# Kernel optimization log

Measured on AMD Instinct MI355X. Metric: run time of the kernel, lower is better.

Reference implementation:

```python
import jax, jax.numpy as jnp
import numpy as np

MIN_NORM = 1e-15
EPS = 1e-7          # fp32 eps used by hgcn Hyperboloid
MAX_NORM = 1e6
C = 1.0             # curvature for all layers (args.c = 1)
N, D = 16384, 64

# ---- Hyperboloid manifold ops (faithful to hgcn manifolds/hyperboloid.py) ----

def _norm(v):
    return jnp.sqrt(jnp.sum(v * v, axis=-1, keepdims=True))

def proj(x, c):
    K = 1.0 / c
    y = x[..., 1:]
    x0 = jnp.sqrt(jnp.clip(K + jnp.sum(y * y, -1, keepdims=True), EPS))
    return jnp.concatenate([x0, y], -1)

def proj_tan0(u, c):
    return jnp.concatenate([jnp.zeros_like(u[..., :1]), u[..., 1:]], -1)

def expmap0(u, c):
    sqrtK = (1.0 / c) ** 0.5
    x = u[..., 1:]
    xn = jnp.clip(_norm(x), MIN_NORM)
    theta = xn / sqrtK
    res = jnp.concatenate([sqrtK * jnp.cosh(theta),
                           sqrtK * jnp.sinh(theta) * x / xn], -1)
    return proj(res, c)

def logmap0(x, c):
    sqrtK = (1.0 / c) ** 0.5
    y = x[..., 1:]
    yn = jnp.clip(_norm(y), MIN_NORM)
    theta = jnp.clip(x[..., :1] / sqrtK, 1.0 + EPS)
    return jnp.concatenate([jnp.zeros_like(theta),
                            sqrtK * jnp.arccosh(theta) * y / yn], -1)

def mink_dot(x, y):
    return -x[..., :1] * y[..., :1] + jnp.sum(x[..., 1:] * y[..., 1:], -1, keepdims=True)

def expmap(u, x, c):
    sqrtK = (1.0 / c) ** 0.5
    normu = jnp.minimum(jnp.sqrt(jnp.clip(mink_dot(u, u), EPS)), MAX_NORM)
    theta = jnp.clip(normu / sqrtK, MIN_NORM)
    return proj(jnp.cosh(theta) * x + jnp.sinh(theta) * u / theta, c)

def proj_tan(u, x, c):
    ux = jnp.sum(x[..., 1:] * u[..., 1:], -1, keepdims=True)
    return jnp.concatenate([ux / jnp.clip(x[..., :1], EPS), u[..., 1:]], -1)

def ptransp0(x, u, c):
    sqrtK = (1.0 / c) ** 0.5
    x0, y = x[..., :1], x[..., 1:]
    yn = jnp.clip(_norm(y), MIN_NORM)
    yhat = y / yn
    v = jnp.concatenate([-yn, (sqrtK - x0) * yhat], -1)
    alpha = jnp.sum(yhat * u[..., 1:], -1, keepdims=True) / sqrtK
    return proj_tan(u - alpha * v, x, c)

def mobius_add(x, y, c):
    u = logmap0(y, c)
    v = ptransp0(x, u, c)
    return expmap(v, x, c)

# ---- HGCN layers (HypLinear -> HypAgg -> HypAct), dropout=0, use_att=False ----

def hyp_linear(x, W, b, c):
    mv = expmap0(logmap0(x, c) @ W.T, c)   # mobius_matvec
    res = proj(mv, c)
    hyp_bias = proj(expmap0(proj_tan0(b[None, :], c), c), c)
    return proj(mobius_add(res, hyp_bias, c), c)

def hyp_agg(x, adj_n, c):
    return proj(expmap0(adj_n @ logmap0(x, c), c), c)

def hyp_act(x, c_in, c_out):
    xt = proj_tan0(jax.nn.relu(logmap0(x, c_in)), c_out)
    return proj(expmap0(xt, c_out), c_out)

def hgc_layer(x, adj_n, W, b, c_in, c_out):
    h = hyp_linear(x, W, b, c_in)
    h = hyp_agg(h, adj_n, c_in)
    return hyp_act(h, c_in, c_out)

def setup_inputs() -> dict:
    key = jax.random.key(0)
    k1, k2, k3, k4, k5, k6 = jax.random.split(key, 6)
    return {
        "x": jax.random.normal(k1, (N, D), jnp.float32),
        "adj": jax.random.uniform(k2, (N, N), jnp.float32),
        "W1": jax.random.normal(k3, (D, D), jnp.float32) * 0.125,
        "b1": jax.random.normal(k4, (D,), jnp.float32) * 0.01,
        "W2": jax.random.normal(k5, (D, D), jnp.float32) * 0.125,
        "b2": jax.random.normal(k6, (D,), jnp.float32) * 0.01,
    }

def reference(x, adj, W1, b1, W2, b2):
    # project input to hyperboloid
    x_hyp = proj(expmap0(proj_tan0(x, C), C), C)
    # row-normalize adjacency: D^{-1} A (inf -> 0)
    rsum = jnp.sum(adj, axis=1)
    rinv = jnp.where(rsum != 0, 1.0 / rsum, 0.0)
    adj_n = rinv[:, None] * adj
    h1 = hgc_layer(x_hyp, adj_n, W1, b1, C, C)
    h2 = hgc_layer(h1, adj_n, W2, b2, C, C)
    return (h1, h2)
```

## Files before the change

### kernel.cpp

```cpp
#include <hip/hip_runtime.h>
#include <cstdint>
#include <cstddef>

#define NROWS 16384
#define KDIM  16384
#define EPSF  1e-7f
#define MINN  1e-15f
#define MAXN  1e6f
#define KSPLIT 8
#define KRANGE (KDIM/KSPLIT)
#define BM    64
#define BK    64
#define NSTEP (KRANGE/BK)
#define APGS  528
#define BPGS  520
#define ABUF  (8*APGS)
#define BBUF  (8*BPGS)

typedef __attribute__((ext_vector_type(16))) float f32x16;
typedef long long i64;
typedef unsigned long long u64;
typedef unsigned int uint;

__device__ __forceinline__ float wredsum(float v){
  v += __shfl_xor(v, 1);
  v += __shfl_xor(v, 2);
  v += __shfl_xor(v, 4);
  v += __shfl_xor(v, 8);
  v += __shfl_xor(v, 16);
  v += __shfl_xor(v, 32);
  return v;
}

__global__ __launch_bounds__(128) void k_bias(const float* __restrict__ b1,
                                              const float* __restrict__ b2,
                                              float* __restrict__ ub){
  int w = threadIdx.x >> 6, l = threadIdx.x & 63;
  const float* b = w ? b2 : b1;
  float bv = b[l];
  float tb = l ? bv : 0.f;
  float s  = wredsum(tb*tb);
  float xn = fmaxf(sqrtf(s), MINN);
  float sc = sinhf(xn)/xn;
  float e  = sc*tb;
  float s2 = wredsum(e*e);
  float x0 = sqrtf(fmaxf(1.f+s2, EPSF));
  float yn = fmaxf(sqrtf(s2), MINN);
  float th = fmaxf(x0, 1.f+EPSF);
  float u  = l ? acoshf(th)*e/yn : 0.f;
  ub[w*64 + l] = u;
}

__global__ __launch_bounds__(256) void k_cvt(const float* __restrict__ adj,
                                             uint* __restrict__ adjF8,
                                             float* __restrict__ rinv){
  int tid  = threadIdx.x;
  int lane = tid & 63;
  int row  = blockIdx.x*4 + (tid >> 6);
  const float4* src = (const float4*)(adj + (size_t)row*KDIM);
  uint* dst = adjF8 + (size_t)row*(KDIM/4);
  float rs = 0.f;
  #pragma unroll 8
  for(int it = 0; it < KDIM/256; it++){
    float4 v = src[it*64 + lane];
    rs += (v.x + v.y) + (v.z + v.w);
    uint p = __builtin_amdgcn_cvt_pk_fp8_f32(v.x, v.y, 0u, false);
    p = __builtin_amdgcn_cvt_pk_fp8_f32(v.z, v.w, p, true);
    dst[it*64 + lane] = p;
  }
  rs = wredsum(rs);
  if (lane == 0) rinv[row] = (rs != 0.f) ? 1.f/rs : 0.f;
}

template<int MODE>
__global__ __launch_bounds__(256) void k_linear(const float* __restrict__ in,
                                                const float* __restrict__ W,
                                                const float* __restrict__ ub,
                                                float* __restrict__ g){
  __shared__ float Wt[64*65];
  int tid = threadIdx.x;
  for(int idx = tid; idx < 4096; idx += 256){
    int j = idx >> 6, k = idx & 63;
    Wt[k*65 + j] = W[idx];
  }
  __syncthreads();
  int lane = tid & 63;
  int row  = blockIdx.x*4 + (tid >> 6);
  float v = in[(size_t)row*64 + lane];
  float lx;
  if (MODE == 0){
    float t  = lane ? v : 0.f;
    float s  = wredsum(t*t);
    float tn = fmaxf(sqrtf(s), MINN);
    float sc = sinhf(tn)/tn;
    float e  = sc*t;
    float s2 = wredsum(e*e);
    float x0 = sqrtf(fmaxf(1.f+s2, EPSF));
    float yn = fmaxf(sqrtf(s2), MINN);
    float th = fmaxf(x0, 1.f+EPSF);
    lx = lane ? acoshf(th)*e/yn : 0.f;
  } else {
    float t  = lane ? v : 0.f;
    float s2 = wredsum(t*t);
    float x0 = __shfl(v, 0);
    float yn = fmaxf(sqrtf(s2), MINN);
    float th = fmaxf(x0, 1.f+EPSF);
    lx = lane ? acoshf(th)*t/yn : 0.f;
  }
  float mv = 0.f;
  #pragma unroll
  for(int k = 0; k < 64; k++){
    mv = fmaf(__shfl(lx, k), Wt[k*65 + lane], mv);
  }
  float u  = lane ? mv : 0.f;
  float s  = wredsum(u*u);
  float un = fmaxf(sqrtf(s), MINN);
  float sc = sinhf(un)/un;
  float e  = sc*u;
  float s2 = wredsum(e*e);
  float r0 = sqrtf(fmaxf(1.f+s2, EPSF));
  float ubt   = lane ? ub[lane] : 0.f;
  float yn    = fmaxf(sqrtf(s2), MINN);
  float yhat  = e/yn;
  float alpha = wredsum(yhat*ubt);
  float w     = ubt - alpha*(1.f - r0)*yhat;
  float ux    = wredsum(e*w);
  float v0    = ux / fmaxf(r0, EPSF);
  float md    = wredsum(w*w) - v0*v0;
  float normu = fminf(sqrtf(fmaxf(md, EPSF)), MAXN);
  float th2   = fmaxf(normu, MINN);
  float ch    = coshf(th2);
  float shq   = sinhf(th2)/th2;
  float ov    = ch*(lane ? e : r0) + shq*(lane ? w : v0);
  float ot    = lane ? ov : 0.f;
  float s3    = wredsum(ot*ot);
  float o0    = sqrtf(fmaxf(1.f+s3, EPSF));
  float yn2 = fmaxf(sqrtf(s3), MINN);
  float th3 = fmaxf(o0, 1.f+EPSF);
  float gv  = lane ? acoshf(th3)*ot/yn2 : 0.f;
  g[(size_t)row*64 + lane] = gv;
}

__global__ __launch_bounds__(256) void k_trf8(const float* __restrict__ g,
                                              uint* __restrict__ gF8T){
  __shared__ float t[64][65];
  int tid = threadIdx.x;
  int b   = blockIdx.x;
  int r   = tid >> 2;
  int c0  = (tid & 3)*16;
  const float* src = g + ((size_t)b*64 + r)*64 + c0;
  #pragma unroll
  for(int i = 0; i < 4; i++){
    float4 v = *(const float4*)(src + i*4);
    t[r][c0 + i*4 + 0] = v.x; t[r][c0 + i*4 + 1] = v.y;
    t[r][c0 + i*4 + 2] = v.z; t[r][c0 + i*4 + 3] = v.w;
  }
  __syncthreads();
  int n   = tid >> 2;
  int seg = tid & 3;
  int s16 = seg*16;
  uint4 p;
  p.x = __builtin_amdgcn_cvt_pk_fp8_f32(t[s16+ 0][n], t[s16+ 1][n], 0u, false);
  p.x = __builtin_amdgcn_cvt_pk_fp8_f32(t[s16+ 2][n], t[s16+ 3][n], p.x, true);
  p.y = __builtin_amdgcn_cvt_pk_fp8_f32(t[s16+ 4][n], t[s16+ 5][n], 0u, false);
  p.y = __builtin_amdgcn_cvt_pk_fp8_f32(t[s16+ 6][n], t[s16+ 7][n], p.y, true);
  p.z = __builtin_amdgcn_cvt_pk_fp8_f32(t[s16+ 8][n], t[s16+ 9][n], 0u, false);
  p.z = __builtin_amdgcn_cvt_pk_fp8_f32(t[s16+10][n], t[s16+11][n], p.z, true);
  p.w = __builtin_amdgcn_cvt_pk_fp8_f32(t[s16+12][n], t[s16+13][n], 0u, false);
  p.w = __builtin_amdgcn_cvt_pk_fp8_f32(t[s16+14][n], t[s16+15][n], p.w, true);
  uint4* dst = (uint4*)gF8T + (size_t)n*(KDIM/16) + b*4 + seg;
  *dst = p;
}

__global__ __launch_bounds__(256) void k_matmul(const unsigned char* __restrict__ adjF8,
                                                const unsigned char* __restrict__ gF8T,
                                                float* __restrict__ pagg){
  __shared__ __align__(16) char Alds[2*ABUF];
  __shared__ __align__(16) char Blds[2*BBUF];
  int tid  = threadIdx.x;
  int lane = tid & 63, w = tid >> 6;
  int rb   = blockIdx.x;
  int ks   = blockIdx.y;
  int row0 = rb*BM;
  size_t k0 = (size_t)ks * KRANGE;

  int sr   = tid >> 2;
  int sseg = tid & 3;
  const uint4* ap = (const uint4*)(adjF8 + (size_t)(row0 + sr)*KDIM + k0 + sseg*16);
  int AwOff0 = (2*sseg    )*APGS + sr*8;
  int AwOff1 = (2*sseg + 1)*APGS + sr*8;

  int sc  = tid >> 2;
  int skq = tid & 3;
  const uint4* bsp = (const uint4*)(gF8T + (size_t)sc*KDIM + k0 + skq*16);
  int BwOff0 = (2*skq    )*BPGS + sc*8;
  int BwOff1 = (2*skq + 1)*BPGS + sc*8;

  int wm = w >> 1, wn = w & 1;
  int lr = lane & 31, lh = lane >> 5;
  int ArdOff = lh*APGS + (wm*32 + lr)*8;
  int BrdOff = lh*BPGS + (wn*32 + lr)*8;

  f32x16 acc;
  #pragma unroll
  for(int q = 0; q < 16; q++) acc[q] = 0.f;

  uint4 aR, aN, bR, bN;

  aR = ap[0];
  bR = bsp[0];
  {
    union { uint4 v; u64 q[2]; } ua; ua.v = aR;
    *(u64*)(Alds + AwOff0) = ua.q[0];
    *(u64*)(Alds + AwOff1) = ua.q[1];
    union { uint4 v; u64 q[2]; } ub_; ub_.v = bR;
    *(u64*)(Blds + BwOff0) = ub_.q[0];
    *(u64*)(Blds + BwOff1) = ub_.q[1];
  }
  aR = ap[4];
  bR = bsp[4];
  __syncthreads();

  for (int i = 0; i < NSTEP; i++){
    const char* Ab = Alds + (i & 1)*ABUF;
    const char* Bb = Blds + (i & 1)*BBUF;
    i64 af0 = *(const i64*)(Ab + ArdOff);
    i64 af1 = *(const i64*)(Ab + ArdOff + 2*APGS);
    i64 af2 = *(const i64*)(Ab + ArdOff + 4*APGS);
    i64 af3 = *(const i64*)(Ab + ArdOff + 6*APGS);
    i64 bf0 = *(const i64*)(Bb + BrdOff);
    i64 bf1 = *(const i64*)(Bb + BrdOff + 2*BPGS);
    i64 bf2 = *(const i64*)(Bb + BrdOff + 4*BPGS);
    i64 bf3 = *(const i64*)(Bb + BrdOff + 6*BPGS);
    if (i + 2 < NSTEP){
      aN = ap[(i+2)*4];
      bN = bsp[(i+2)*4];
    }
    acc = __builtin_amdgcn_mfma_f32_32x32x16_fp8_fp8(af0, bf0, acc, 0, 0, 0);
    acc = __builtin_amdgcn_mfma_f32_32x32x16_fp8_fp8(af1, bf1, acc, 0, 0, 0);
    acc = __builtin_amdgcn_mfma_f32_32x32x16_fp8_fp8(af2, bf2, acc, 0, 0, 0);
    acc = __builtin_amdgcn_mfma_f32_32x32x16_fp8_fp8(af3, bf3, acc, 0, 0, 0);
    if (i + 1 < NSTEP){
      char* Aw = Alds + ((i+1) & 1)*ABUF;
      char* Bw = Blds + ((i+1) & 1)*BBUF;
      union { uint4 v; u64 q[2]; } ua; ua.v = aR;
      *(u64*)(Aw + AwOff0) = ua.q[0];
      *(u64*)(Aw + AwOff1) = ua.q[1];
      union { uint4 v; u64 q[2]; } ub_; ub_.v = bR;
      *(u64*)(Bw + BwOff0) = ub_.q[0];
      *(u64*)(Bw + BwOff1) = ub_.q[1];
    }
    aR = aN; bR = bN;
    __syncthreads();
  }

  float* ob = pagg + ((size_t)ks*NROWS + row0 + wm*32)*64 + wn*32;
  #pragma unroll
  for(int q = 0; q < 16; q++){
    int rl = (q & 3) + 8*(q >> 2) + 4*lh;
    ob[(size_t)rl*64 + lr] = acc[q];
  }
}

__global__ __launch_bounds__(256) void k_post(const float* __restrict__ pagg,
                                              const float* __restrict__ rinv,
                                              float* __restrict__ h){
  int tid = threadIdx.x; int lane = tid & 63;
  int row = blockIdx.x*4 + (tid >> 6);
  float s = 0.f;
  #pragma unroll
  for(int ks = 0; ks < KSPLIT; ks++) s += pagg[(size_t)ks*NROWS*64 + (size_t)row*64 + lane];
  float a  = s * rinv[row];
  float at = lane ? a : 0.f;
  float ss = wredsum(at*at);
  float un = fmaxf(sqrtf(ss), MINN);
  float sc = sinhf(un)/un;
  float e  = sc*at;
  float s2 = wredsum(e*e);
  float x0 = sqrtf(fmaxf(1.f+s2, EPSF));
  float yn = fmaxf(sqrtf(s2), MINN);
  float th = fmaxf(x0, 1.f+EPSF);
  float lt = lane ? acoshf(th)*e/yn : 0.f;
  float rl = fmaxf(lt, 0.f);
  float s3 = wredsum(rl*rl);
  float rn = fmaxf(sqrtf(s3), MINN);
  float sc2= sinhf(rn)/rn;
  float e2 = sc2*rl;
  float s4 = wredsum(e2*e2);
  float h0 = sqrtf(fmaxf(1.f+s4, EPSF));
  h[(size_t)row*64 + lane] = lane ? e2 : h0;
}

extern "C" void kernel_launch(void* const* d_in, const int* in_sizes, int n_in,
                              void* d_out, int out_size, void* d_ws, size_t ws_size,
                              hipStream_t stream){
  const float* x   = (const float*)d_in[0];
  const float* adj = (const float*)d_in[1];
  const float* W1  = (const float*)d_in[2];
  const float* b1  = (const float*)d_in[3];
  const float* W2  = (const float*)d_in[4];
  const float* b2  = (const float*)d_in[5];
  float* out = (float*)d_out;
  float* h1  = out;
  float* h2  = out + (size_t)NROWS*64;

  float* wsf   = (float*)d_ws;
  float* gbuf  = wsf;
  float* pagg  = gbuf  + (size_t)NROWS*64;
  float* rinv  = pagg  + (size_t)KSPLIT*NROWS*64;
  float* ubs   = rinv  + NROWS;
  uint*  gF8T  = (uint*)(ubs + 128);
  uint*  adjF8 = gF8T + (size_t)64*KDIM/4;

  dim3 gm(NROWS/BM, KSPLIT);

  k_bias<<<1, 128, 0, stream>>>(b1, b2, ubs);
  k_cvt<<<NROWS/4, 256, 0, stream>>>(adj, adjF8, rinv);
  k_linear<0><<<NROWS/4, 256, 0, stream>>>(x, W1, ubs, gbuf);
  k_trf8<<<NROWS/64, 256, 0, stream>>>(gbuf, gF8T);
  k_matmul<<<gm, 256, 0, stream>>>((const unsigned char*)adjF8, (const unsigned char*)gF8T, pagg);
  k_post<<<NROWS/4, 256, 0, stream>>>(pagg, rinv, h1);
  k_linear<1><<<NROWS/4, 256, 0, stream>>>(h1, W2, ubs + 64, gbuf);
  k_trf8<<<NROWS/64, 256, 0, stream>>>(gbuf, gF8T);
  k_matmul<<<gm, 256, 0, stream>>>((const unsigned char*)adjF8, (const unsigned char*)gF8T, pagg);
  k_post<<<NROWS/4, 256, 0, stream>>>(pagg, rinv, h2);
}
```

Before: 521.9 us.

## Fuse fp32-to-fp8 adjacency conversion and row sums into first aggregation matmul

Removes the standalone conversion kernel. The first matmul now reads fp32 adjacency directly, converts each tile to fp8 in registers, writes the fp8 copy out for reuse by the second layer, and accumulates partial row sums. The first post kernel reduces these partial sums to get the row normalizers. The second matmul walks its blocks in reverse order, so it starts on the adjacency tiles the first one touched last and may still find them in cache. This saves one full pass reading the 1 GB fp32 adjacency, but puts conversion work and larger fp32 loads inside the matmul's pipeline.

```diff
diff --git a/kernel.cpp b/kernel.cpp
--- a/kernel.cpp
+++ b/kernel.cpp
@@ -12,6 +12,7 @@
 #define BM    64
 #define BK    64
 #define NSTEP (KRANGE/BK)
+#define NRB   (NROWS/BM)
 #define APGS  528
 #define BPGS  520
 #define ABUF  (8*APGS)
@@ -49,27 +50,6 @@
   float th = fmaxf(x0, 1.f+EPSF);
   float u  = l ? acoshf(th)*e/yn : 0.f;
   ub[w*64 + l] = u;
-}
-
-__global__ __launch_bounds__(256) void k_cvt(const float* __restrict__ adj,
-                                             uint* __restrict__ adjF8,
-                                             float* __restrict__ rinv){
-  int tid  = threadIdx.x;
-  int lane = tid & 63;
-  int row  = blockIdx.x*4 + (tid >> 6);
-  const float4* src = (const float4*)(adj + (size_t)row*KDIM);
-  uint* dst = adjF8 + (size_t)row*(KDIM/4);
-  float rs = 0.f;
-  #pragma unroll 8
-  for(int it = 0; it < KDIM/256; it++){
-    float4 v = src[it*64 + lane];
-    rs += (v.x + v.y) + (v.z + v.w);
-    uint p = __builtin_amdgcn_cvt_pk_fp8_f32(v.x, v.y, 0u, false);
-    p = __builtin_amdgcn_cvt_pk_fp8_f32(v.z, v.w, p, true);
-    dst[it*64 + lane] = p;
-  }
-  rs = wredsum(rs);
-  if (lane == 0) rinv[row] = (rs != 0.f) ? 1.f/rs : 0.f;
 }
 
 template<int MODE>
@@ -172,15 +152,145 @@
   *dst = p;
 }
 
-__global__ __launch_bounds__(256) void k_matmul(const unsigned char* __restrict__ adjF8,
-                                                const unsigned char* __restrict__ gF8T,
-                                                float* __restrict__ pagg){
+__global__ __launch_bounds__(256) void k_matmul1(const float* __restrict__ adj,
+                                                 const unsigned char* __restrict__ gF8T,
+                                                 float* __restrict__ pagg,
+                                                 float* __restrict__ prsum,
+                                                 uint* __restrict__ adjF8){
   __shared__ __align__(16) char Alds[2*ABUF];
   __shared__ __align__(16) char Blds[2*BBUF];
   int tid  = threadIdx.x;
   int lane = tid & 63, w = tid >> 6;
   int rb   = blockIdx.x;
   int ks   = blockIdx.y;
+  int row0 = rb*BM;
+  size_t k0 = (size_t)ks * KRANGE;
+
+  int sr   = tid >> 2;
+  int sseg = tid & 3;
+  const float4* ap = (const float4*)(adj + (size_t)(row0 + sr)*KDIM + k0) + sseg*4;
+  uint* aw = adjF8 + ((size_t)(row0 + sr)*KDIM + k0)/4 + sseg*4;
+  int AwOff0 = (2*sseg    )*APGS + sr*8;
+  int AwOff1 = (2*sseg + 1)*APGS + sr*8;
+
+  int sc  = tid >> 2;
+  int skq = tid & 3;
+  const uint4* bsp = (const uint4*)(gF8T + (size_t)sc*KDIM + k0 + skq*16);
+  int BwOff0 = (2*skq    )*BPGS + sc*8;
+  int BwOff1 = (2*skq + 1)*BPGS + sc*8;
+
+  int wm = w >> 1, wn = w & 1;
+  int lr = lane & 31, lh = lane >> 5;
+  int ArdOff = lh*APGS + (wm*32 + lr)*8;
+  int BrdOff = lh*BPGS + (wn*32 + lr)*8;
+
+  f32x16 acc;
+  #pragma unroll
+  for(int q = 0; q < 16; q++) acc[q] = 0.f;
+  float rs = 0.f;
+
+  float4 aR[4], aN[4];
+  uint4 bR, bN;
+
+  #pragma unroll
+  for(int q = 0; q < 4; q++) aR[q] = ap[q];
+  bR = bsp[0];
+  {
+    #pragma unroll
+    for(int q = 0; q < 4; q++) rs += aR[q].x + aR[q].y + aR[q].z + aR[q].w;
+    uint4 ak;
+    ak.x = __builtin_amdgcn_cvt_pk_fp8_f32(aR[0].x, aR[0].y, 0u, false);
+    ak.x = __builtin_amdgcn_cvt_pk_fp8_f32(aR[0].z, aR[0].w, ak.x, true);
+    ak.y = __builtin_amdgcn_cvt_pk_fp8_f32(aR[1].x, aR[1].y, 0u, false);
+    ak.y = __builtin_amdgcn_cvt_pk_fp8_f32(aR[1].z, aR[1].w, ak.y, true);
+    ak.z = __builtin_amdgcn_cvt_pk_fp8_f32(aR[2].x, aR[2].y, 0u, false);
+    ak.z = __builtin_amdgcn_cvt_pk_fp8_f32(aR[2].z, aR[2].w, ak.z, true);
+    ak.w = __builtin_amdgcn_cvt_pk_fp8_f32(aR[3].x, aR[3].y, 0u, false);
+    ak.w = __builtin_amdgcn_cvt_pk_fp8_f32(aR[3].z, aR[3].w, ak.w, true);
+    *(uint4*)(aw) = ak;
+    union { uint4 v; u64 q[2]; } ua; ua.v = ak;
+    *(u64*)(Alds + AwOff0) = ua.q[0];
+    *(u64*)(Alds + AwOff1) = ua.q[1];
+    union { uint4 v; u64 q[2]; } ub_; ub_.v = bR;
+    *(u64*)(Blds + BwOff0) = ub_.q[0];
+    *(u64*)(Blds + BwOff1) = ub_.q[1];
+  }
+  #pragma unroll
+  for(int q = 0; q < 4; q++) aR[q] = ap[16 + q];
+  bR = bsp[4];
+  __syncthreads();
+
+  for (int i = 0; i < NSTEP; i++){
+    const char* Ab = Alds + (i & 1)*ABUF;
+    const char* Bb = Blds + (i & 1)*BBUF;
+    i64 af0 = *(const i64*)(Ab + ArdOff);
+    i64 af1 = *(const i64*)(Ab + ArdOff + 2*APGS);
+    i64 af2 = *(const i64*)(Ab + ArdOff + 4*APGS);
+    i64 af3 = *(const i64*)(Ab + ArdOff + 6*APGS);
+    i64 bf0 = *(const i64*)(Bb + BrdOff);
+    i64 bf1 = *(const i64*)(Bb + BrdOff + 2*BPGS);
+    i64 bf2 = *(const i64*)(Bb + BrdOff + 4*BPGS);
+    i64 bf3 = *(const i64*)(Bb + BrdOff + 6*BPGS);
+    uint4 ak;
+    if (i + 1 < NSTEP){
+      #pragma unroll
+      for(int q = 0; q < 4; q++) rs += aR[q].x + aR[q].y + aR[q].z + aR[q].w;
+      ak.x = __builtin_amdgcn_cvt_pk_fp8_f32(aR[0].x, aR[0].y, 0u, false);
+      ak.x = __builtin_amdgcn_cvt_pk_fp8_f32(aR[0].z, aR[0].w, ak.x, true);
+      ak.y = __builtin_amdgcn_cvt_pk_fp8_f32(aR[1].x, aR[1].y, 0u, false);
+      ak.y = __builtin_amdgcn_cvt_pk_fp8_f32(aR[1].z, aR[1].w, ak.y, true);
+      ak.z = __builtin_amdgcn_cvt_pk_fp8_f32(aR[2].x, aR[2].y, 0u, false);
+      ak.z = __builtin_amdgcn_cvt_pk_fp8_f32(aR[2].z, aR[2].w, ak.z, true);
+      ak.w = __builtin_amdgcn_cvt_pk_fp8_f32(aR[3].x, aR[3].y, 0u, false);
+      ak.w = __builtin_amdgcn_cvt_pk_fp8_f32(aR[3].z, aR[3].w, ak.w, true);
+      *(uint4*)(aw + (size_t)(i+1)*16) = ak;
+    }
+    if (i + 2 < NSTEP){
+      #pragma unroll
+      for(int q = 0; q < 4; q++) aN[q] = ap[(i+2)*16 + q];
+      bN = bsp[(i+2)*4];
+    }
+    acc = __builtin_amdgcn_mfma_f32_32x32x16_fp8_fp8(af0, bf0, acc, 0, 0, 0);
+    acc = __builtin_amdgcn_mfma_f32_32x32x16_fp8_fp8(af1, bf1, acc, 0, 0, 0);
+    acc = __builtin_amdgcn_mfma_f32_32x32x16_fp8_fp8(af2, bf2, acc, 0, 0, 0);
+    acc = __builtin_amdgcn_mfma_f32_32x32x16_fp8_fp8(af3, bf3, acc, 0, 0, 0);
+    if (i + 1 < NSTEP){
+      char* Aw = Alds + ((i+1) & 1)*ABUF;
+      char* Bw = Blds + ((i+1) & 1)*BBUF;
+      union { uint4 v; u64 q[2]; } ua; ua.v = ak;
+      *(u64*)(Aw + AwOff0) = ua.q[0];
+      *(u64*)(Aw + AwOff1) = ua.q[1];
+      union { uint4 v; u64 q[2]; } ub_; ub_.v = bR;
+      *(u64*)(Bw + BwOff0) = ub_.q[0];
+      *(u64*)(Bw + BwOff1) = ub_.q[1];
+    }
+    #pragma unroll
+    for(int q = 0; q < 4; q++) aR[q] = aN[q];
+    bR = bN;
+    __syncthreads();
+  }
+
+  rs += __shfl_xor(rs, 1);
+  rs += __shfl_xor(rs, 2);
+  if ((lane & 3) == 0) prsum[(size_t)ks*NROWS + row0 + sr] = rs;
+
+  float* ob = pagg + ((size_t)ks*NROWS + row0 + wm*32)*64 + wn*32;
+  #pragma unroll
+  for(int q = 0; q < 16; q++){
+    int rl = (q & 3) + 8*(q >> 2) + 4*lh;
+    ob[(size_t)rl*64 + lr] = acc[q];
+  }
+}
+
+__global__ __launch_bounds__(256) void k_matmul2(const unsigned char* __restrict__ adjF8,
+                                                 const unsigned char* __restrict__ gF8T,
+                                                 float* __restrict__ pagg){
+  __shared__ __align__(16) char Alds[2*ABUF];
+  __shared__ __align__(16) char Blds[2*BBUF];
+  int tid  = threadIdx.x;
+  int lane = tid & 63, w = tid >> 6;
+  int rb   = NRB - 1 - blockIdx.x;
+  int ks   = KSPLIT - 1 - blockIdx.y;
   int row0 = rb*BM;
   size_t k0 = (size_t)ks * KRANGE;
 
@@ -262,15 +372,27 @@
   }
 }
 
+template<int LAYER>
 __global__ __launch_bounds__(256) void k_post(const float* __restrict__ pagg,
-                                              const float* __restrict__ rinv,
+                                              const float* __restrict__ prsum,
+                                              float* __restrict__ rinv,
                                               float* __restrict__ h){
   int tid = threadIdx.x; int lane = tid & 63;
   int row = blockIdx.x*4 + (tid >> 6);
   float s = 0.f;
   #pragma unroll
   for(int ks = 0; ks < KSPLIT; ks++) s += pagg[(size_t)ks*NROWS*64 + (size_t)row*64 + lane];
-  float a  = s * rinv[row];
+  float ri;
+  if (LAYER == 1){
+    float rsum = 0.f;
+    #pragma unroll
+    for(int ks = 0; ks < KSPLIT; ks++) rsum += prsum[(size_t)ks*NROWS + row];
+    ri = (rsum != 0.f) ? 1.f/rsum : 0.f;
+    if (lane == 0) rinv[row] = ri;
+  } else {
+    ri = rinv[row];
+  }
+  float a  = s * ri;
   float at = lane ? a : 0.f;
   float ss = wredsum(at*at);
   float un = fmaxf(sqrtf(ss), MINN);
@@ -307,21 +429,21 @@
   float* wsf   = (float*)d_ws;
   float* gbuf  = wsf;
   float* pagg  = gbuf  + (size_t)NROWS*64;
-  float* rinv  = pagg  + (size_t)KSPLIT*NROWS*64;
+  float* prsum = pagg  + (size_t)KSPLIT*NROWS*64;
+  float* rinv  = prsum + (size_t)KSPLIT*NROWS;
   float* ubs   = rinv  + NROWS;
   uint*  gF8T  = (uint*)(ubs + 128);
   uint*  adjF8 = gF8T + (size_t)64*KDIM/4;
 
-  dim3 gm(NROWS/BM, KSPLIT);
+  dim3 gm(NRB, KSPLIT);
 
   k_bias<<<1, 128, 0, stream>>>(b1, b2, ubs);
-  k_cvt<<<NROWS/4, 256, 0, stream>>>(adj, adjF8, rinv);
   k_linear<0><<<NROWS/4, 256, 0, stream>>>(x, W1, ubs, gbuf);
   k_trf8<<<NROWS/64, 256, 0, stream>>>(gbuf, gF8T);
-  k_matmul<<<gm, 256, 0, stream>>>((const unsigned char*)adjF8, (const unsigned char*)gF8T, pagg);
-  k_post<<<NROWS/4, 256, 0, stream>>>(pagg, rinv, h1);
+  k_matmul1<<<gm, 256, 0, stream>>>(adj, (const unsigned char*)gF8T, pagg, prsum, adjF8);
+  k_post<1><<<NROWS/4, 256, 0, stream>>>(pagg, prsum, rinv, h1);
   k_linear<1><<<NROWS/4, 256, 0, stream>>>(h1, W2, ubs + 64, gbuf);
   k_trf8<<<NROWS/64, 256, 0, stream>>>(gbuf, gF8T);
-  k_matmul<<<gm, 256, 0, stream>>>((const unsigned char*)adjF8, (const unsigned char*)gF8T, pagg);
-  k_post<<<NROWS/4, 256, 0, stream>>>(pagg, rinv, h2);
-}
+  k_matmul2<<<gm, 256, 0, stream>>>((const unsigned char*)adjF8, (const unsigned char*)gF8T, pagg);
+  k_post<2><<<NROWS/4, 256, 0, stream>>>(pagg, prsum, rinv, h2);
+}
```

Measured after the change: 526.2 us. About the same (+0.8%).

## Fuse linear, post and transpose kernels; halve K-split; unroll conversion loop

Applied to the files above, without the earlier changes.

Merges the hyperbolic linear stage with the fp8 transpose, and the post-aggregation activation with the next layer's linear and transpose, into single kernels that stage results in shared memory. This removes the fp32 intermediate buffer round-trip through global memory and several launches. KSPLIT drops from 8 to 4, halving the partial-sum traffic but giving the matmul fewer blocks. The adjacency conversion loop is manually unrolled by four for more memory-level parallelism. The fused kernels process 16 rows per wave serially, with 4x fewer blocks, which lowers parallelism in those stages.

```diff
diff --git a/kernel.cpp b/kernel.cpp
--- a/kernel.cpp
+++ b/kernel.cpp
@@ -7,11 +7,12 @@
 #define EPSF  1e-7f
 #define MINN  1e-15f
 #define MAXN  1e6f
-#define KSPLIT 8
+#define KSPLIT 4
 #define KRANGE (KDIM/KSPLIT)
 #define BM    64
 #define BK    64
 #define NSTEP (KRANGE/BK)
+#define NRB   (NROWS/BM)
 #define APGS  528
 #define BPGS  520
 #define ABUF  (8*APGS)
@@ -60,33 +61,34 @@
   const float4* src = (const float4*)(adj + (size_t)row*KDIM);
   uint* dst = adjF8 + (size_t)row*(KDIM/4);
   float rs = 0.f;
-  #pragma unroll 8
-  for(int it = 0; it < KDIM/256; it++){
-    float4 v = src[it*64 + lane];
-    rs += (v.x + v.y) + (v.z + v.w);
-    uint p = __builtin_amdgcn_cvt_pk_fp8_f32(v.x, v.y, 0u, false);
-    p = __builtin_amdgcn_cvt_pk_fp8_f32(v.z, v.w, p, true);
-    dst[it*64 + lane] = p;
+  for(int it = 0; it < 16; it++){
+    float4 v0 = src[(it*4+0)*64 + lane];
+    float4 v1 = src[(it*4+1)*64 + lane];
+    float4 v2 = src[(it*4+2)*64 + lane];
+    float4 v3 = src[(it*4+3)*64 + lane];
+    rs += (v0.x+v0.y)+(v0.z+v0.w) + (v1.x+v1.y)+(v1.z+v1.w)
+        + (v2.x+v2.y)+(v2.z+v2.w) + (v3.x+v3.y)+(v3.z+v3.w);
+    uint p0 = __builtin_amdgcn_cvt_pk_fp8_f32(v0.x, v0.y, 0u, false);
+    p0 = __builtin_amdgcn_cvt_pk_fp8_f32(v0.z, v0.w, p0, true);
+    uint p1 = __builtin_amdgcn_cvt_pk_fp8_f32(v1.x, v1.y, 0u, false);
+    p1 = __builtin_amdgcn_cvt_pk_fp8_f32(v1.z, v1.w, p1, true);
+    uint p2 = __builtin_amdgcn_cvt_pk_fp8_f32(v2.x, v2.y, 0u, false);
+    p2 = __builtin_amdgcn_cvt_pk_fp8_f32(v2.z, v2.w, p2, true);
+    uint p3 = __builtin_amdgcn_cvt_pk_fp8_f32(v3.x, v3.y, 0u, false);
+    p3 = __builtin_amdgcn_cvt_pk_fp8_f32(v3.z, v3.w, p3, true);
+    dst[(it*4+0)*64 + lane] = p0;
+    dst[(it*4+1)*64 + lane] = p1;
+    dst[(it*4+2)*64 + lane] = p2;
+    dst[(it*4+3)*64 + lane] = p3;
   }
   rs = wredsum(rs);
   if (lane == 0) rinv[row] = (rs != 0.f) ? 1.f/rs : 0.f;
 }
 
 template<int MODE>
-__global__ __launch_bounds__(256) void k_linear(const float* __restrict__ in,
-                                                const float* __restrict__ W,
-                                                const float* __restrict__ ub,
-                                                float* __restrict__ g){
-  __shared__ float Wt[64*65];
-  int tid = threadIdx.x;
-  for(int idx = tid; idx < 4096; idx += 256){
-    int j = idx >> 6, k = idx & 63;
-    Wt[k*65 + j] = W[idx];
-  }
-  __syncthreads();
-  int lane = tid & 63;
-  int row  = blockIdx.x*4 + (tid >> 6);
-  float v = in[(size_t)row*64 + lane];
+__device__ __forceinline__ float lin_chain(float v, int lane,
+                                           const float* __restrict__ Wt,
+                                           const float* __restrict__ ub){
   float lx;
   if (MODE == 0){
     float t  = lane ? v : 0.f;
@@ -137,39 +139,94 @@
   float o0    = sqrtf(fmaxf(1.f+s3, EPSF));
   float yn2 = fmaxf(sqrtf(s3), MINN);
   float th3 = fmaxf(o0, 1.f+EPSF);
-  float gv  = lane ? acoshf(th3)*ot/yn2 : 0.f;
-  g[(size_t)row*64 + lane] = gv;
-}
-
-__global__ __launch_bounds__(256) void k_trf8(const float* __restrict__ g,
-                                              uint* __restrict__ gF8T){
-  __shared__ float t[64][65];
-  int tid = threadIdx.x;
-  int b   = blockIdx.x;
-  int r   = tid >> 2;
-  int c0  = (tid & 3)*16;
-  const float* src = g + ((size_t)b*64 + r)*64 + c0;
-  #pragma unroll
-  for(int i = 0; i < 4; i++){
-    float4 v = *(const float4*)(src + i*4);
-    t[r][c0 + i*4 + 0] = v.x; t[r][c0 + i*4 + 1] = v.y;
-    t[r][c0 + i*4 + 2] = v.z; t[r][c0 + i*4 + 3] = v.w;
-  }
-  __syncthreads();
+  return lane ? acoshf(th3)*ot/yn2 : 0.f;
+}
+
+__device__ __forceinline__ void tr_out(const float (*gt)[65], int tid, int blk,
+                                       uint* __restrict__ gF8T){
   int n   = tid >> 2;
   int seg = tid & 3;
   int s16 = seg*16;
   uint4 p;
-  p.x = __builtin_amdgcn_cvt_pk_fp8_f32(t[s16+ 0][n], t[s16+ 1][n], 0u, false);
-  p.x = __builtin_amdgcn_cvt_pk_fp8_f32(t[s16+ 2][n], t[s16+ 3][n], p.x, true);
-  p.y = __builtin_amdgcn_cvt_pk_fp8_f32(t[s16+ 4][n], t[s16+ 5][n], 0u, false);
-  p.y = __builtin_amdgcn_cvt_pk_fp8_f32(t[s16+ 6][n], t[s16+ 7][n], p.y, true);
-  p.z = __builtin_amdgcn_cvt_pk_fp8_f32(t[s16+ 8][n], t[s16+ 9][n], 0u, false);
-  p.z = __builtin_amdgcn_cvt_pk_fp8_f32(t[s16+10][n], t[s16+11][n], p.z, true);
-  p.w = __builtin_amdgcn_cvt_pk_fp8_f32(t[s16+12][n], t[s16+13][n], 0u, false);
-  p.w = __builtin_amdgcn_cvt_pk_fp8_f32(t[s16+14][n], t[s16+15][n], p.w, true);
-  uint4* dst = (uint4*)gF8T + (size_t)n*(KDIM/16) + b*4 + seg;
+  p.x = __builtin_amdgcn_cvt_pk_fp8_f32(gt[s16+ 0][n], gt[s16+ 1][n], 0u, false);
+  p.x = __builtin_amdgcn_cvt_pk_fp8_f32(gt[s16+ 2][n], gt[s16+ 3][n], p.x, true);
+  p.y = __builtin_amdgcn_cvt_pk_fp8_f32(gt[s16+ 4][n], gt[s16+ 5][n], 0u, false);
+  p.y = __builtin_amdgcn_cvt_pk_fp8_f32(gt[s16+ 6][n], gt[s16+ 7][n], p.y, true);
+  p.z = __builtin_amdgcn_cvt_pk_fp8_f32(gt[s16+ 8][n], gt[s16+ 9][n], 0u, false);
+  p.z = __builtin_amdgcn_cvt_pk_fp8_f32(gt[s16+10][n], gt[s16+11][n], p.z, true);
+  p.w = __builtin_amdgcn_cvt_pk_fp8_f32(gt[s16+12][n], gt[s16+13][n], 0u, false);
+  p.w = __builtin_amdgcn_cvt_pk_fp8_f32(gt[s16+14][n], gt[s16+15][n], p.w, true);
+  uint4* dst = (uint4*)gF8T + (size_t)n*(KDIM/16) + blk*4 + seg;
   *dst = p;
+}
+
+__global__ __launch_bounds__(256) void k_lin0(const float* __restrict__ x,
+                                              const float* __restrict__ W,
+                                              const float* __restrict__ ub,
+                                              uint* __restrict__ gF8T){
+  __shared__ float Wt[64*65];
+  __shared__ float gt[64][65];
+  int tid = threadIdx.x;
+  for(int idx = tid; idx < 4096; idx += 256){
+    int j = idx >> 6, k = idx & 63;
+    Wt[k*65 + j] = W[idx];
+  }
+  __syncthreads();
+  int lane = tid & 63, w = tid >> 6;
+  int rbase = blockIdx.x*64 + w*16;
+  for(int rr = 0; rr < 16; rr++){
+    float v = x[(size_t)(rbase + rr)*64 + lane];
+    gt[w*16 + rr][lane] = lin_chain<0>(v, lane, Wt, ub);
+  }
+  __syncthreads();
+  tr_out(gt, tid, blockIdx.x, gF8T);
+}
+
+__global__ __launch_bounds__(256) void k_mid(const float* __restrict__ pagg,
+                                             const float* __restrict__ rinv,
+                                             const float* __restrict__ W,
+                                             const float* __restrict__ ub,
+                                             float* __restrict__ h,
+                                             uint* __restrict__ gF8T){
+  __shared__ float Wt[64*65];
+  __shared__ float gt[64][65];
+  int tid = threadIdx.x;
+  for(int idx = tid; idx < 4096; idx += 256){
+    int j = idx >> 6, k = idx & 63;
+    Wt[k*65 + j] = W[idx];
+  }
+  __syncthreads();
+  int lane = tid & 63, w = tid >> 6;
+  int rbase = blockIdx.x*64 + w*16;
+  for(int rr = 0; rr < 16; rr++){
+    int row = rbase + rr;
+    float s = 0.f;
+    #pragma unroll
+    for(int ks = 0; ks < KSPLIT; ks++) s += pagg[(size_t)ks*NROWS*64 + (size_t)row*64 + lane];
+    float a  = s * rinv[row];
+    float at = lane ? a : 0.f;
+    float ss = wredsum(at*at);
+    float un = fmaxf(sqrtf(ss), MINN);
+    float sc = sinhf(un)/un;
+    float e  = sc*at;
+    float s2 = wredsum(e*e);
+    float x0 = sqrtf(fmaxf(1.f+s2, EPSF));
+    float yn = fmaxf(sqrtf(s2), MINN);
+    float th = fmaxf(x0, 1.f+EPSF);
+    float lt = lane ? acoshf(th)*e/yn : 0.f;
+    float rl = fmaxf(lt, 0.f);
+    float s3 = wredsum(rl*rl);
+    float rn = fmaxf(sqrtf(s3), MINN);
+    float sc2= sinhf(rn)/rn;
+    float e2 = sc2*rl;
+    float s4 = wredsum(e2*e2);
+    float h0 = sqrtf(fmaxf(1.f+s4, EPSF));
+    float hv = lane ? e2 : h0;
+    h[(size_t)row*64 + lane] = hv;
+    gt[w*16 + rr][lane] = lin_chain<1>(hv, lane, Wt, ub);
+  }
+  __syncthreads();
+  tr_out(gt, tid, blockIdx.x, gF8T);
 }
 
 __global__ __launch_bounds__(256) void k_matmul(const unsigned char* __restrict__ adjF8,
@@ -262,9 +319,9 @@
   }
 }
 
-__global__ __launch_bounds__(256) void k_post(const float* __restrict__ pagg,
-                                              const float* __restrict__ rinv,
-                                              float* __restrict__ h){
+__global__ __launch_bounds__(256) void k_post2(const float* __restrict__ pagg,
+                                               const float* __restrict__ rinv,
+                                               float* __restrict__ h){
   int tid = threadIdx.x; int lane = tid & 63;
   int row = blockIdx.x*4 + (tid >> 6);
   float s = 0.f;
@@ -305,23 +362,19 @@
   float* h2  = out + (size_t)NROWS*64;
 
   float* wsf   = (float*)d_ws;
-  float* gbuf  = wsf;
-  float* pagg  = gbuf  + (size_t)NROWS*64;
+  float* pagg  = wsf;
   float* rinv  = pagg  + (size_t)KSPLIT*NROWS*64;
   float* ubs   = rinv  + NROWS;
   uint*  gF8T  = (uint*)(ubs + 128);
   uint*  adjF8 = gF8T + (size_t)64*KDIM/4;
 
-  dim3 gm(NROWS/BM, KSPLIT);
+  dim3 gm(NRB, KSPLIT);
 
   k_bias<<<1, 128, 0, stream>>>(b1, b2, ubs);
   k_cvt<<<NROWS/4, 256, 0, stream>>>(adj, adjF8, rinv);
-  k_linear<0><<<NROWS/4, 256, 0, stream>>>(x, W1, ubs, gbuf);
-  k_trf8<<<NROWS/64, 256, 0, stream>>>(gbuf, gF8T);
+  k_lin0<<<NROWS/64, 256, 0, stream>>>(x, W1, ubs, gF8T);
   k_matmul<<<gm, 256, 0, stream>>>((const unsigned char*)adjF8, (const unsigned char*)gF8T, pagg);
-  k_post<<<NROWS/4, 256, 0, stream>>>(pagg, rinv, h1);
-  k_linear<1><<<NROWS/4, 256, 0, stream>>>(h1, W2, ubs + 64, gbuf);
-  k_trf8<<<NROWS/64, 256, 0, stream>>>(gbuf, gF8T);
+  k_mid<<<NROWS/64, 256, 0, stream>>>(pagg, rinv, W2, ubs + 64, h1, gF8T);
   k_matmul<<<gm, 256, 0, stream>>>((const unsigned char*)adjF8, (const unsigned char*)gF8T, pagg);
-  k_post<<<NROWS/4, 256, 0, stream>>>(pagg, rinv, h2);
-}
+  k_post2<<<NROWS/4, 256, 0, stream>>>(pagg, rinv, h2);
+}
```

Measured after the change: 616.0 us. +18.0%, slower.
